# Kernel optimization log

Hardware: AMD Instinct MI355X
Metric: run time of the kernel (lower is better)

Reference implementation:

```python
import jax, jax.numpy as jnp
import numpy as np

DROPOUT_RATE = 0.1  # init arg dropout_rate
B, D, N_SEL = 4096, 4096, 2048


def setup_inputs() -> dict:
    key = jax.random.key(0)
    k1, k2 = jax.random.split(key)
    inputs = jax.random.normal(k1, (B, D), dtype=jnp.float32)
    neuron_indices = jax.random.randint(k2, (N_SEL,), 0, D, dtype=jnp.int32)
    return {"inputs": inputs, "neuron_indices": neuron_indices}


def reference(inputs, neuron_indices):
    # Training-mode SelectiveDropout: for each listed neuron (column), draw an
    # independent uniform; drop the column (0) with prob p, else scale by 1/(1-p).
    # Unlisted columns keep scale 1. Vectorized replacement for the per-index
    # torch.rand(1) loop.
    key = jax.random.key(42)
    u = jax.random.uniform(key, neuron_indices.shape, dtype=jnp.float32)
    keep_scale = jnp.where(u < DROPOUT_RATE, 0.0, 1.0 / (1.0 - DROPOUT_RATE))
    scale = jnp.ones((inputs.shape[1],), dtype=inputs.dtype)
    scale = scale.at[neuron_indices].set(keep_scale.astype(inputs.dtype))
    return inputs * scale[None, :]
```

## Files before the change

kernel.cpp:

```cpp
#include <hip/hip_runtime.h>
#include <stdint.h>


#define THREEFRY_PARTITIONABLE 1
#define D_DIM 4096

__device__ __forceinline__ uint32_t rotl32(uint32_t v, uint32_t n) {
  return (v << n) | (v >> (32u - n));
}

__device__ __forceinline__ void threefry2x32(uint32_t x0, uint32_t x1,
                                             uint32_t& o0, uint32_t& o1) {
  const uint32_t ks0 = 0u;
  const uint32_t ks1 = 42u;
  const uint32_t ks2 = 0u ^ 42u ^ 0x1BD11BDAu;

  x0 += ks0;
  x1 += ks1;

#define TF_GROUP(a, b, c, d)                           \
  x0 += x1; x1 = rotl32(x1, a); x1 ^= x0;              \
  x0 += x1; x1 = rotl32(x1, b); x1 ^= x0;              \
  x0 += x1; x1 = rotl32(x1, c); x1 ^= x0;              \
  x0 += x1; x1 = rotl32(x1, d); x1 ^= x0;

  TF_GROUP(13, 15, 26, 6)  x0 += ks1; x1 += ks2 + 1u;
  TF_GROUP(17, 29, 16, 24) x0 += ks2; x1 += ks0 + 2u;
  TF_GROUP(13, 15, 26, 6)  x0 += ks0; x1 += ks1 + 3u;
  TF_GROUP(17, 29, 16, 24) x0 += ks1; x1 += ks2 + 4u;
  TF_GROUP(13, 15, 26, 6)  x0 += ks2; x1 += ks0 + 5u;
#undef TF_GROUP

  o0 = x0;
  o1 = x1;
}

__device__ __forceinline__ float jax_uniform_at(int i, int n) {
  uint32_t bits;
#if THREEFRY_PARTITIONABLE
  uint32_t o0, o1;
  threefry2x32(0u, (uint32_t)i, o0, o1);
  bits = o0 ^ o1;
#else
  int half = n >> 1;
  uint32_t o0, o1;
  if (i < half) {
    threefry2x32((uint32_t)i, (uint32_t)(i + half), o0, o1);
    bits = o0;
  } else {
    threefry2x32((uint32_t)(i - half), (uint32_t)i, o0, o1);
    bits = o1;
  }
#endif
  uint32_t fb = (bits >> 9) | 0x3F800000u;
  return __uint_as_float(fb) - 1.0f;
}

__global__ __launch_bounds__(1024) void build_scale_kernel(
    const int* __restrict__ idx, int n, float* __restrict__ scale_g) {
  __shared__ int winner[D_DIM];
  __shared__ float sc[D_DIM];
  const int t = threadIdx.x;

  for (int d = t; d < D_DIM; d += 1024) {
    winner[d] = -1;
    sc[d] = 1.0f;
  }
  __syncthreads();

  for (int i = t; i < n; i += 1024) {
    atomicMax(&winner[idx[i]], i);
  }
  __syncthreads();

  const float inv_keep = (float)(1.0 / (1.0 - 0.1));
  for (int i = t; i < n; i += 1024) {
    int col = idx[i];
    if (winner[col] == i) {
      float u = jax_uniform_at(i, n);
      sc[col] = (u < 0.1f) ? 0.0f : inv_keep;
    }
  }
  __syncthreads();

  for (int d = t; d < D_DIM; d += 1024) {
    scale_g[d] = sc[d];
  }
}

__global__ __launch_bounds__(256) void apply_scale_kernel(
    const float4* __restrict__ in, const float4* __restrict__ scale4,
    float4* __restrict__ out, int total4) {
  const int stride = gridDim.x * blockDim.x;
  for (int e = blockIdx.x * blockDim.x + threadIdx.x; e < total4; e += stride) {
    float4 v = in[e];
    float4 s = scale4[e & 1023];
    v.x *= s.x;
    v.y *= s.y;
    v.z *= s.z;
    v.w *= s.w;
    out[e] = v;
  }
}

extern "C" void kernel_launch(void* const* d_in, const int* in_sizes, int n_in,
                              void* d_out, int out_size, void* d_ws, size_t ws_size,
                              hipStream_t stream) {
  const float* in = (const float*)d_in[0];
  const int* idx = (const int*)d_in[1];
  float* out = (float*)d_out;
  float* scale = (float*)d_ws;

  const int n_idx = in_sizes[1];
  const int total = in_sizes[0];
  const int total4 = total / 4;

  hipLaunchKernelGGL(build_scale_kernel, dim3(1), dim3(1024), 0, stream,
                     idx, n_idx, scale);

  const int blocks = 2048;
  hipLaunchKernelGGL(apply_scale_kernel, dim3(blocks), dim3(256), 0, stream,
                     (const float4*)in, (const float4*)scale, (float4*)out,
                     total4);
}
```

Measured before the change: 30.23 us.

## Pack winner index with keep bit and unroll nontemporal scale apply

The scale builder now computes the random keep bit for every index and packs it with the index into one atomicMax. That removes the second pass, one shared array and a barrier. The apply kernel adds a fast path for when the total equals eight times the stride: it hoists the scale load, issues eight independent nontemporal loads per thread, then does nontemporal stores. The goal is more memory-level parallelism and less cache pollution in the bandwidth-bound streaming pass, at the cost of running threefry for every index, including duplicates.

```diff
diff --git a/kernel.cpp b/kernel.cpp
--- a/kernel.cpp
+++ b/kernel.cpp
@@ -2,8 +2,9 @@
 #include <stdint.h>
 
 
-#define THREEFRY_PARTITIONABLE 1
 #define D_DIM 4096
+
+typedef float f32x4 __attribute__((ext_vector_type(4)));
 
 __device__ __forceinline__ uint32_t rotl32(uint32_t v, uint32_t n) {
   return (v << n) | (v >> (32u - n));
@@ -35,71 +36,64 @@
   o1 = x1;
 }
 
-__device__ __forceinline__ float jax_uniform_at(int i, int n) {
-  uint32_t bits;
-#if THREEFRY_PARTITIONABLE
+__device__ __forceinline__ float jax_uniform_at(int i) {
   uint32_t o0, o1;
   threefry2x32(0u, (uint32_t)i, o0, o1);
-  bits = o0 ^ o1;
-#else
-  int half = n >> 1;
-  uint32_t o0, o1;
-  if (i < half) {
-    threefry2x32((uint32_t)i, (uint32_t)(i + half), o0, o1);
-    bits = o0;
-  } else {
-    threefry2x32((uint32_t)(i - half), (uint32_t)i, o0, o1);
-    bits = o1;
-  }
-#endif
+  uint32_t bits = o0 ^ o1;
   uint32_t fb = (bits >> 9) | 0x3F800000u;
   return __uint_as_float(fb) - 1.0f;
 }
 
 __global__ __launch_bounds__(1024) void build_scale_kernel(
-    const int* __restrict__ idx, int n, float* __restrict__ scale_g) {
-  __shared__ int winner[D_DIM];
-  __shared__ float sc[D_DIM];
+    const int* __restrict__ idx, int n, f32x4* __restrict__ scale_g) {
+  __shared__ int packed[D_DIM];
   const int t = threadIdx.x;
 
-  for (int d = t; d < D_DIM; d += 1024) {
-    winner[d] = -1;
-    sc[d] = 1.0f;
-  }
+  for (int d = t; d < D_DIM; d += 1024) packed[d] = -1;
   __syncthreads();
 
   for (int i = t; i < n; i += 1024) {
-    atomicMax(&winner[idx[i]], i);
+    int col = idx[i];
+    float u = jax_uniform_at(i);
+    int keep = (u < 0.1f) ? 0 : 1;
+    atomicMax(&packed[col], (i << 1) | keep);
   }
   __syncthreads();
 
   const float inv_keep = (float)(1.0 / (1.0 - 0.1));
-  for (int i = t; i < n; i += 1024) {
-    int col = idx[i];
-    if (winner[col] == i) {
-      float u = jax_uniform_at(i, n);
-      sc[col] = (u < 0.1f) ? 0.0f : inv_keep;
+  for (int d4 = t; d4 < D_DIM / 4; d4 += 1024) {
+    f32x4 s;
+    for (int j = 0; j < 4; ++j) {
+      int p = packed[d4 * 4 + j];
+      s[j] = (p < 0) ? 1.0f : ((p & 1) ? inv_keep : 0.0f);
     }
-  }
-  __syncthreads();
-
-  for (int d = t; d < D_DIM; d += 1024) {
-    scale_g[d] = sc[d];
+    scale_g[d4] = s;
   }
 }
 
 __global__ __launch_bounds__(256) void apply_scale_kernel(
-    const float4* __restrict__ in, const float4* __restrict__ scale4,
-    float4* __restrict__ out, int total4) {
-  const int stride = gridDim.x * blockDim.x;
-  for (int e = blockIdx.x * blockDim.x + threadIdx.x; e < total4; e += stride) {
-    float4 v = in[e];
-    float4 s = scale4[e & 1023];
-    v.x *= s.x;
-    v.y *= s.y;
-    v.z *= s.z;
-    v.w *= s.w;
-    out[e] = v;
+    const f32x4* __restrict__ in, const f32x4* __restrict__ scale4,
+    f32x4* __restrict__ out, int total4) {
+  const int tid = blockIdx.x * 256 + threadIdx.x;
+  const int stride = gridDim.x * 256;
+
+  if (total4 == stride * 8) {
+    const f32x4 s = scale4[tid & 1023];
+    f32x4 v[8];
+#pragma unroll
+    for (int k = 0; k < 8; ++k)
+      v[k] = __builtin_nontemporal_load(&in[tid + k * stride]);
+#pragma unroll
+    for (int k = 0; k < 8; ++k) {
+      v[k] *= s;
+      __builtin_nontemporal_store(v[k], &out[tid + k * stride]);
+    }
+  } else {
+    for (int e = tid; e < total4; e += stride) {
+      f32x4 v = in[e];
+      v *= scale4[e & 1023];
+      out[e] = v;
+    }
   }
 }
 
@@ -116,10 +110,10 @@
   const int total4 = total / 4;
 
   hipLaunchKernelGGL(build_scale_kernel, dim3(1), dim3(1024), 0, stream,
-                     idx, n_idx, scale);
+                     idx, n_idx, (f32x4*)scale);
 
   const int blocks = 2048;
   hipLaunchKernelGGL(apply_scale_kernel, dim3(blocks), dim3(256), 0, stream,
-                     (const float4*)in, (const float4*)scale, (float4*)out,
+                     (const f32x4*)in, (const f32x4*)scale, (f32x4*)out,
                      total4);
 }
```

Measured after the change: 36.92 us. 1.22x slower.
